# Kernel tuning notes

Measured on AMD Instinct MI355X. Metric: run time of the kernel, lower is better.

Reference implementation:

```python
import jax, jax.numpy as jnp
import numpy as np

N_NODES = 100000
IN_F = 32
OUT_F = 32
EDGE_F = 16
N_EDGES = 400000
BN_EPS = 1e-5
LEAKY_SLOPE = 0.01


def setup_inputs() -> dict:
    key = jax.random.key(0)
    ks = jax.random.split(key, 8)
    node_feature = jax.random.normal(ks[0], (N_NODES, IN_F), dtype=jnp.float32)
    edge_feature = jax.random.normal(ks[1], (N_EDGES, EDGE_F), dtype=jnp.float32)
    nn_w = jax.random.normal(ks[2], (EDGE_F, IN_F * OUT_F), dtype=jnp.float32) * (1.0 / np.sqrt(EDGE_F))
    nn_b = jax.random.normal(ks[3], (IN_F * OUT_F,), dtype=jnp.float32) * 0.01
    root = jax.random.normal(ks[4], (IN_F, OUT_F), dtype=jnp.float32) * (1.0 / np.sqrt(IN_F))
    bias = jax.random.normal(ks[5], (OUT_F,), dtype=jnp.float32) * 0.01
    gamma = jnp.ones((OUT_F,), dtype=jnp.float32)
    beta = jnp.zeros((OUT_F,), dtype=jnp.float32)
    edge_index = jax.random.randint(ks[6], (2, N_EDGES), 0, N_NODES, dtype=jnp.int64)
    return {
        "node_feature": node_feature,
        "edge_feature": edge_feature,
        "nn_w": nn_w,
        "nn_b": nn_b,
        "root": root,
        "bias": bias,
        "gamma": gamma,
        "beta": beta,
        "edge_index": edge_index,
    }


def reference(node_feature, edge_feature, nn_w, nn_b, root, bias, gamma, beta, edge_index):
    src, dst = edge_index[0], edge_index[1]  # messages flow src -> dst (PyG source_to_target)
    # Edge MLP: per-edge weight matrix [E, IN_F, OUT_F]
    edge_w = (edge_feature @ nn_w + nn_b).reshape(-1, IN_F, OUT_F)
    # Gather source node features and apply per-edge matmul: [E, OUT_F]
    msg = jnp.einsum("ei,eio->eo", node_feature[src], edge_w)
    # Scatter-add aggregation at target nodes
    agg = jax.ops.segment_sum(msg, dst, num_segments=node_feature.shape[0])
    # Root transform + bias (NNConv root_weight=True, bias=True)
    h = agg + node_feature @ root + bias
    # BatchNorm1d (training mode: batch statistics over nodes, biased variance)
    mean = jnp.mean(h, axis=0)
    var = jnp.var(h, axis=0)
    h = (h - mean) * jax.lax.rsqrt(var + BN_EPS) * gamma + beta
    # LeakyReLU (default negative_slope = 0.01)
    return jnp.where(h >= 0, h, LEAKY_SLOPE * h)
```

## Files before the change

### kernel.cpp

```cpp
#include <hip/hip_runtime.h>

#define IN_F 32
#define OUT_F 32
#define EDGE_F 16
#define BN_EPS 1e-5f
#define SLOPE 0.01f

typedef _Float16 half_t;
typedef __attribute__((ext_vector_type(4))) _Float16 h4;
typedef __attribute__((ext_vector_type(8))) _Float16 f16x8;
typedef __attribute__((ext_vector_type(4))) float f32x4;

#define BCOLS 576
#define BSTRIDE_B 80

__global__ __launch_bounds__(256) void prep_bt_kernel(
    const float* __restrict__ W, const float* __restrict__ b,
    const float* __restrict__ root, half_t* __restrict__ BtG) {
  int idx = blockIdx.x * 256 + threadIdx.x;
  if (idx >= BCOLS * 32) return;
  int o = idx & 31;
  int k = (idx >> 5) & 31;
  int fp = idx >> 10;
  float v;
  int col;
  if (fp < 16) {
    v = W[(size_t)fp * 1024 + k * 32 + o];
    col = fp * 32 + o;
  } else if (fp == 16) {
    v = b[k * 32 + o];
    col = 512 + o;
  } else {
    v = root[k * 32 + o];
    col = 544 + o;
  }
  BtG[(size_t)col * 32 + k] = (half_t)v;
}

__global__ __launch_bounds__(256) void gemm_y_mfma_kernel(
    const float* __restrict__ x, const half_t* __restrict__ BtG,
    const float* __restrict__ bias, half_t* __restrict__ Y,
    float* __restrict__ out, int N) {
  __shared__ char BtL[BCOLS * BSTRIDE_B];

  int tid = threadIdx.x;
  for (int t = tid; t < BCOLS * 4; t += 256) {
    int col = t >> 2, part = t & 3;
    *(float4*)(BtL + col * BSTRIDE_B + part * 16) =
        *(const float4*)((const char*)BtG + col * 64 + part * 16);
  }
  __syncthreads();

  int wv = tid >> 6, lane = tid & 63;
  int lr = lane & 15, kg = lane >> 4;
  int n0 = blockIdx.x * 64 + wv * 16;
  int row = n0 + lr;

  f16x8 a;
  if (row < N) {
    float4 u0 = *(const float4*)(x + (size_t)row * 32 + kg * 8);
    float4 u1 = *(const float4*)(x + (size_t)row * 32 + kg * 8 + 4);
    a[0] = (half_t)u0.x; a[1] = (half_t)u0.y; a[2] = (half_t)u0.z; a[3] = (half_t)u0.w;
    a[4] = (half_t)u1.x; a[5] = (half_t)u1.y; a[6] = (half_t)u1.z; a[7] = (half_t)u1.w;
  } else {
    a = (f16x8)(half_t)0.f;
  }

  for (int ct = 0; ct < 36; ++ct) {
    int col = ct * 16 + lr;
    f16x8 bf = *(const f16x8*)(BtL + col * BSTRIDE_B + kg * 16);
    f32x4 c = {0.f, 0.f, 0.f, 0.f};
    c = __builtin_amdgcn_mfma_f32_16x16x32_f16(a, bf, c, 0, 0, 0);
    if (col < 544) {
#pragma unroll
      for (int j = 0; j < 4; ++j) {
        int n = n0 + kg * 4 + j;
        if (n < N) Y[(size_t)n * 544 + col] = (half_t)c[j];
      }
    } else {
      int o = col - 544;
      float bv = bias[o];
#pragma unroll
      for (int j = 0; j < 4; ++j) {
        int n = n0 + kg * 4 + j;
        if (n < N) out[(size_t)n * OUT_F + o] = c[j] + bv;
      }
    }
  }
}

__global__ __launch_bounds__(256) void edge_light_kernel(
    const half_t* __restrict__ Y, const float* __restrict__ ef,
    const int* __restrict__ ei, float* __restrict__ agg, int E) {
  __shared__ float efl[32][17];
  __shared__ float msg[32][33];
  __shared__ int dstl[32];

  int e0 = blockIdx.x * 32;
  int t = threadIdx.x;
  int el = t >> 3, oq = t & 7;
  int e = e0 + el;
  bool ev = (e < E);
  int s = ev ? ei[e] : 0;

  const half_t* yrow = Y + (size_t)s * 544 + oq * 4;
  h4 yv[17];
#pragma unroll
  for (int f = 0; f < 17; ++f) yv[f] = *(const h4*)(yrow + f * 32);
  __builtin_amdgcn_sched_barrier(0);

  if (t < 128) {
    int ee = e0 + (t >> 2);
    int q = t & 3;
    float4 v = make_float4(0.f, 0.f, 0.f, 0.f);
    if (ee < E) v = *(const float4*)(ef + (size_t)ee * EDGE_F + q * 4);
    efl[t >> 2][q * 4 + 0] = v.x; efl[t >> 2][q * 4 + 1] = v.y;
    efl[t >> 2][q * 4 + 2] = v.z; efl[t >> 2][q * 4 + 3] = v.w;
  }
  if (t < 32) {
    int ee = e0 + t;
    dstl[t] = (ee < E) ? ei[E + ee] : -1;
  }
  __syncthreads();

  float acc[4];
#pragma unroll
  for (int j = 0; j < 4; ++j) acc[j] = (float)yv[16][j];
#pragma unroll
  for (int f = 0; f < EDGE_F; ++f) {
    float m = efl[el][f];
#pragma unroll
    for (int j = 0; j < 4; ++j) acc[j] = fmaf(m, (float)yv[f][j], acc[j]);
  }
#pragma unroll
  for (int j = 0; j < 4; ++j) msg[el][oq * 4 + j] = acc[j];
  __syncthreads();

  int d = dstl[el];
  if (d >= 0) {
    float* dp = agg + (size_t)d * OUT_F;
#pragma unroll
    for (int j = 0; j < 4; ++j)
      atomicAdd(dp + j * 8 + oq, msg[el][j * 8 + oq]);
  }
}

__global__ __launch_bounds__(256) void node_root_kernel(
    const float* __restrict__ x, const float* __restrict__ root,
    const float* __restrict__ bias, float* __restrict__ agg, int N) {
  __shared__ float rl[IN_F * OUT_F];
  __shared__ float bl[OUT_F];
  for (int t = threadIdx.x; t < IN_F * OUT_F; t += blockDim.x) rl[t] = root[t];
  if (threadIdx.x < OUT_F) bl[threadIdx.x] = bias[threadIdx.x];
  __syncthreads();
  int n = blockIdx.x * blockDim.x + threadIdx.x;
  bool valid = (n < N);
  int nu = valid ? n : 0;
  float xr[IN_F];
  const float4* xp = (const float4*)(x + (size_t)nu * IN_F);
#pragma unroll
  for (int q = 0; q < IN_F / 4; ++q) {
    float4 v = xp[q];
    xr[q * 4 + 0] = v.x; xr[q * 4 + 1] = v.y; xr[q * 4 + 2] = v.z; xr[q * 4 + 3] = v.w;
  }
  float acc[OUT_F];
#pragma unroll
  for (int o = 0; o < OUT_F; ++o) acc[o] = bl[o];
#pragma unroll
  for (int i = 0; i < IN_F; ++i) {
    float xi = xr[i];
#pragma unroll
    for (int o = 0; o < OUT_F; ++o) acc[o] = fmaf(xi, rl[i * OUT_F + o], acc[o]);
  }
  if (valid) {
    float4* op = (float4*)(agg + (size_t)n * OUT_F);
#pragma unroll
    for (int q = 0; q < OUT_F / 4; ++q)
      op[q] = make_float4(acc[q * 4 + 0], acc[q * 4 + 1], acc[q * 4 + 2], acc[q * 4 + 3]);
  }
}

__global__ __launch_bounds__(256) void edge_kernel(
    const float* __restrict__ x, const float* __restrict__ ef,
    const float* __restrict__ W, const float* __restrict__ b,
    const int* __restrict__ ei, float* __restrict__ agg, int E) {
  __shared__ float Wl[EDGE_F * IN_F * OUT_F];
  int e = blockIdx.x * blockDim.x + threadIdx.x;
  bool valid = (e < E);
  int eu = valid ? e : 0;
  int s = ei[eu];
  int d = ei[E + eu];
  float efr[EDGE_F];
  {
    const float4* ep = (const float4*)(ef + (size_t)eu * EDGE_F);
#pragma unroll
    for (int q = 0; q < EDGE_F / 4; ++q) {
      float4 v = ep[q];
      efr[q * 4 + 0] = v.x; efr[q * 4 + 1] = v.y;
      efr[q * 4 + 2] = v.z; efr[q * 4 + 3] = v.w;
    }
  }
  const float* xrow = x + (size_t)s * IN_F;
  float acc[OUT_F];
#pragma unroll
  for (int o = 0; o < OUT_F; ++o) acc[o] = 0.f;
  for (int t = threadIdx.x; t < IN_F * OUT_F; t += 256) Wl[t] = b[t];
  __syncthreads();
  for (int i = 0; i < IN_F; ++i) {
    float xi = xrow[i];
    const float* br = &Wl[i * OUT_F];
#pragma unroll
    for (int o = 0; o < OUT_F; ++o) acc[o] = fmaf(xi, br[o], acc[o]);
  }
  __syncthreads();
  for (int t = threadIdx.x; t < EDGE_F * IN_F * OUT_F / 4; t += 256)
    ((float4*)Wl)[t] = ((const float4*)W)[t];
  __syncthreads();
  for (int i = 0; i < IN_F; ++i) {
    float xi = xrow[i];
#pragma unroll
    for (int f = 0; f < EDGE_F; ++f) {
      float m = efr[f] * xi;
      const float* wr = &Wl[(f * IN_F + i) * OUT_F];
#pragma unroll
      for (int o = 0; o < OUT_F; ++o) acc[o] = fmaf(m, wr[o], acc[o]);
    }
  }
  if (valid) {
    float* dp = agg + (size_t)d * OUT_F;
#pragma unroll
    for (int o = 0; o < OUT_F; ++o) atomicAdd(dp + o, acc[o]);
  }
}

__global__ __launch_bounds__(256) void bn_stats_kernel(
    const float* __restrict__ h, float* __restrict__ stats, int total) {
  int t = blockIdx.x * blockDim.x + threadIdx.x;
  int stride = gridDim.x * blockDim.x;
  float s = 0.f, s2 = 0.f;
  for (int idx = t; idx < total; idx += stride) {
    float v = h[idx];
    s += v;
    s2 = fmaf(v, v, s2);
  }
  __shared__ float ls[256], ls2[256];
  ls[threadIdx.x] = s;
  ls2[threadIdx.x] = s2;
  __syncthreads();
  if (threadIdx.x < 32) {
    float a = ls[threadIdx.x], a2 = ls2[threadIdx.x];
    for (int j = 32 + threadIdx.x; j < 256; j += 32) { a += ls[j]; a2 += ls2[j]; }
    atomicAdd(&stats[threadIdx.x], a);
    atomicAdd(&stats[32 + threadIdx.x], a2);
  }
}

__global__ __launch_bounds__(256) void bn_apply_kernel(
    float* __restrict__ h, const float* __restrict__ stats,
    const float* __restrict__ gamma, const float* __restrict__ beta,
    int total, float invN) {
  int t = blockIdx.x * blockDim.x + threadIdx.x;
  int i4 = t * 4;
  if (i4 >= total) return;
  float4 v = *(const float4*)(h + i4);
  float r[4] = {v.x, v.y, v.z, v.w};
  int o0 = i4 & 31;
#pragma unroll
  for (int j = 0; j < 4; ++j) {
    int o = o0 + j;
    float m = stats[o] * invN;
    float var = fmaf(-m, m, stats[32 + o] * invN);
    float sc = rsqrtf(var + BN_EPS) * gamma[o];
    float val = (r[j] - m) * sc + beta[o];
    r[j] = val >= 0.f ? val : SLOPE * val;
  }
  *(float4*)(h + i4) = make_float4(r[0], r[1], r[2], r[3]);
}

extern "C" void kernel_launch(void* const* d_in, const int* in_sizes, int n_in,
                              void* d_out, int out_size, void* d_ws, size_t ws_size,
                              hipStream_t stream) {
  const float* x     = (const float*)d_in[0];
  const float* ef    = (const float*)d_in[1];
  const float* W     = (const float*)d_in[2];
  const float* b     = (const float*)d_in[3];
  const float* root  = (const float*)d_in[4];
  const float* bias  = (const float*)d_in[5];
  const float* gamma = (const float*)d_in[6];
  const float* beta  = (const float*)d_in[7];
  const int*   ei    = (const int*)d_in[8];

  float* out = (float*)d_out;
  float* stats = (float*)d_ws;
  half_t* BtG = (half_t*)((char*)d_ws + 1024);
  half_t* Y = (half_t*)((char*)d_ws + 1024 + 36864);

  int N = in_sizes[0] / IN_F;
  int E = in_sizes[1] / EDGE_F;
  int total = N * OUT_F;
  size_t need = 1024 + 36864 + (size_t)N * 544 * sizeof(half_t);

  hipMemsetAsync(stats, 0, 64 * sizeof(float), stream);

  if (ws_size >= need) {
    prep_bt_kernel<<<(BCOLS * 32 + 255) / 256, 256, 0, stream>>>(W, b, root, BtG);
    gemm_y_mfma_kernel<<<(N + 63) / 64, 256, 0, stream>>>(x, BtG, bias, Y, out, N);
    edge_light_kernel<<<(E + 31) / 32, 256, 0, stream>>>(Y, ef, ei, out, E);
  } else {
    node_root_kernel<<<(N + 255) / 256, 256, 0, stream>>>(x, root, bias, out, N);
    edge_kernel<<<(E + 255) / 256, 256, 0, stream>>>(x, ef, W, b, ei, out, E);
  }
  bn_stats_kernel<<<1024, 256, 0, stream>>>(out, stats, total);
  bn_apply_kernel<<<(total / 4 + 255) / 256, 256, 0, stream>>>(out, stats, gamma, beta, total, 1.0f / (float)N);
}
```

Baseline: 180.3 us.

## Bucket-sort edges by source node and remap blocks across XCDs for gather locality

After: 242.2 us. 1.34x slower.

```diff
diff --git a/kernel.cpp b/kernel.cpp
--- a/kernel.cpp
+++ b/kernel.cpp
@@ -5,6 +5,7 @@
 #define EDGE_F 16
 #define BN_EPS 1e-5f
 #define SLOPE 0.01f
+#define NBUCKET 128
 
 typedef _Float16 half_t;
 typedef __attribute__((ext_vector_type(4))) _Float16 h4;
@@ -16,7 +17,12 @@
 
 __global__ __launch_bounds__(256) void prep_bt_kernel(
     const float* __restrict__ W, const float* __restrict__ b,
-    const float* __restrict__ root, half_t* __restrict__ BtG) {
+    const float* __restrict__ root, half_t* __restrict__ BtG,
+    float* __restrict__ stats, int* __restrict__ hist) {
+  if (blockIdx.x == 0) {
+    if (threadIdx.x < 64) stats[threadIdx.x] = 0.f;
+    else if (threadIdx.x < 64 + NBUCKET) hist[threadIdx.x - 64] = 0;
+  }
   int idx = blockIdx.x * 256 + threadIdx.x;
   if (idx >= BCOLS * 32) return;
   int o = idx & 31;
@@ -37,6 +43,49 @@
   BtG[(size_t)col * 32 + k] = (half_t)v;
 }
 
+__global__ __launch_bounds__(256) void hist_kernel(
+    const int* __restrict__ ei, int* __restrict__ hist, int E, int shift) {
+  __shared__ int lh[NBUCKET];
+  if (threadIdx.x < NBUCKET) lh[threadIdx.x] = 0;
+  __syncthreads();
+  int e = blockIdx.x * 256 + threadIdx.x;
+  if (e < E) atomicAdd(&lh[ei[e] >> shift], 1);
+  __syncthreads();
+  if (threadIdx.x < NBUCKET && lh[threadIdx.x] > 0)
+    atomicAdd(&hist[threadIdx.x], lh[threadIdx.x]);
+}
+
+__global__ __launch_bounds__(256) void scan_kernel(
+    const int* __restrict__ hist, int* __restrict__ cursor) {
+  if (threadIdx.x == 0) {
+    int acc = 0;
+    for (int i = 0; i < NBUCKET; ++i) {
+      cursor[i] = acc;
+      acc += hist[i];
+    }
+  }
+}
+
+__global__ __launch_bounds__(256) void scatter_kernel(
+    const int* __restrict__ ei, int* __restrict__ cursor,
+    int* __restrict__ perm, int E, int shift) {
+  __shared__ int lh[NBUCKET];
+  __shared__ int lbase[NBUCKET];
+  if (threadIdx.x < NBUCKET) lh[threadIdx.x] = 0;
+  __syncthreads();
+  int e = blockIdx.x * 256 + threadIdx.x;
+  int bkt = 0, rank = 0;
+  if (e < E) {
+    bkt = ei[e] >> shift;
+    rank = atomicAdd(&lh[bkt], 1);
+  }
+  __syncthreads();
+  if (threadIdx.x < NBUCKET && lh[threadIdx.x] > 0)
+    lbase[threadIdx.x] = atomicAdd(&cursor[threadIdx.x], lh[threadIdx.x]);
+  __syncthreads();
+  if (e < E) perm[lbase[bkt] + rank] = e;
+}
+
 __global__ __launch_bounds__(256) void gemm_y_mfma_kernel(
     const float* __restrict__ x, const half_t* __restrict__ BtG,
     const float* __restrict__ bias, half_t* __restrict__ Y,
@@ -91,17 +140,24 @@
 
 __global__ __launch_bounds__(256) void edge_light_kernel(
     const half_t* __restrict__ Y, const float* __restrict__ ef,
-    const int* __restrict__ ei, float* __restrict__ agg, int E) {
+    const int* __restrict__ ei, const int* __restrict__ perm,
+    float* __restrict__ agg, int E) {
+  int nwg = gridDim.x;
+  int xcd = blockIdx.x & 7, off = blockIdx.x >> 3;
+  int q = nwg >> 3, r = nwg & 7;
+  int bid = (xcd < r) ? xcd * (q + 1) + off : r * (q + 1) + (xcd - r) * q + off;
+
   __shared__ float efl[32][17];
   __shared__ float msg[32][33];
   __shared__ int dstl[32];
 
-  int e0 = blockIdx.x * 32;
+  int e0 = bid * 32;
   int t = threadIdx.x;
   int el = t >> 3, oq = t & 7;
   int e = e0 + el;
   bool ev = (e < E);
-  int s = ev ? ei[e] : 0;
+  int pe = ev ? perm[e] : 0;
+  int s = ev ? ei[pe] : 0;
 
   const half_t* yrow = Y + (size_t)s * 544 + oq * 4;
   h4 yv[17];
@@ -110,16 +166,16 @@
   __builtin_amdgcn_sched_barrier(0);
 
   if (t < 128) {
-    int ee = e0 + (t >> 2);
-    int q = t & 3;
+    int ep = e0 + (t >> 2);
+    int qq = t & 3;
     float4 v = make_float4(0.f, 0.f, 0.f, 0.f);
-    if (ee < E) v = *(const float4*)(ef + (size_t)ee * EDGE_F + q * 4);
-    efl[t >> 2][q * 4 + 0] = v.x; efl[t >> 2][q * 4 + 1] = v.y;
-    efl[t >> 2][q * 4 + 2] = v.z; efl[t >> 2][q * 4 + 3] = v.w;
+    if (ep < E) v = *(const float4*)(ef + (size_t)perm[ep] * EDGE_F + qq * 4);
+    efl[t >> 2][qq * 4 + 0] = v.x; efl[t >> 2][qq * 4 + 1] = v.y;
+    efl[t >> 2][qq * 4 + 2] = v.z; efl[t >> 2][qq * 4 + 3] = v.w;
   }
   if (t < 32) {
-    int ee = e0 + t;
-    dstl[t] = (ee < E) ? ei[E + ee] : -1;
+    int ep = e0 + t;
+    dstl[t] = (ep < E) ? ei[E + perm[ep]] : -1;
   }
   __syncthreads();
 
@@ -290,23 +346,34 @@
   const float* beta  = (const float*)d_in[7];
   const int*   ei    = (const int*)d_in[8];
 
-  float* out = (float*)d_out;
-  float* stats = (float*)d_ws;
-  half_t* BtG = (half_t*)((char*)d_ws + 1024);
-  half_t* Y = (half_t*)((char*)d_ws + 1024 + 36864);
-
   int N = in_sizes[0] / IN_F;
   int E = in_sizes[1] / EDGE_F;
   int total = N * OUT_F;
-  size_t need = 1024 + 36864 + (size_t)N * 544 * sizeof(half_t);
-
-  hipMemsetAsync(stats, 0, 64 * sizeof(float), stream);
+
+  float* out = (float*)d_out;
+  char* wsb = (char*)d_ws;
+  float*  stats  = (float*)wsb;
+  half_t* BtG    = (half_t*)(wsb + 1024);
+  int*    hist   = (int*)(wsb + 1024 + 36864);
+  int*    cursor = (int*)(wsb + 1024 + 36864 + 512);
+  int*    perm   = (int*)(wsb + 1024 + 36864 + 1024);
+  size_t yoff = 1024 + 36864 + 1024 + (((size_t)E * 4 + 1023) & ~(size_t)1023);
+  half_t* Y = (half_t*)(wsb + yoff);
+
+  int shift = 10;
+  while (((N - 1) >> shift) >= NBUCKET) ++shift;
+
+  size_t need = yoff + (size_t)N * 544 * sizeof(half_t);
 
   if (ws_size >= need) {
-    prep_bt_kernel<<<(BCOLS * 32 + 255) / 256, 256, 0, stream>>>(W, b, root, BtG);
+    prep_bt_kernel<<<(BCOLS * 32 + 255) / 256, 256, 0, stream>>>(W, b, root, BtG, stats, hist);
+    hist_kernel<<<(E + 255) / 256, 256, 0, stream>>>(ei, hist, E, shift);
+    scan_kernel<<<1, 256, 0, stream>>>(hist, cursor);
+    scatter_kernel<<<(E + 255) / 256, 256, 0, stream>>>(ei, cursor, perm, E, shift);
     gemm_y_mfma_kernel<<<(N + 63) / 64, 256, 0, stream>>>(x, BtG, bias, Y, out, N);
-    edge_light_kernel<<<(E + 31) / 32, 256, 0, stream>>>(Y, ef, ei, out, E);
+    edge_light_kernel<<<(E + 31) / 32, 256, 0, stream>>>(Y, ef, ei, perm, out, E);
   } else {
+    hipMemsetAsync(stats, 0, 64 * sizeof(float), stream);
     node_root_kernel<<<(N + 255) / 256, 256, 0, stream>>>(x, root, bias, out, N);
     edge_kernel<<<(E + 255) / 256, 256, 0, stream>>>(x, ef, W, b, ei, out, E);
   }
```

## Replace atomic scatter with CSR-sorted gather aggregation and coalesced GEMM stores

Applied to the files above, without the earlier changes.

Result: slower. 222.3 us (+23.3%).

```diff
diff --git a/kernel.cpp b/kernel.cpp
--- a/kernel.cpp
+++ b/kernel.cpp
@@ -37,11 +37,65 @@
   BtG[(size_t)col * 32 + k] = (half_t)v;
 }
 
+__global__ __launch_bounds__(256) void histd_kernel(
+    const int* __restrict__ ei, int* __restrict__ cnt, int E) {
+  int e = blockIdx.x * 256 + threadIdx.x;
+  if (e < E) atomicAdd(&cnt[ei[E + e]], 1);
+}
+
+__global__ __launch_bounds__(256) void scan_a_kernel(
+    const int* __restrict__ cnt, int* __restrict__ rp, int* __restrict__ bsum, int N) {
+  __shared__ int lds[256];
+  int i = blockIdx.x * 256 + threadIdx.x;
+  int v = (i < N) ? cnt[i] : 0;
+  lds[threadIdx.x] = v;
+  __syncthreads();
+  int ex = 0;
+  for (int j = 0; j < threadIdx.x; ++j) ex += lds[j];
+  if (i < N) rp[i] = ex;
+  if (threadIdx.x == 255) bsum[blockIdx.x] = ex + v;
+}
+
+__global__ __launch_bounds__(512) void scan_b_kernel(
+    const int* __restrict__ bsum, int* __restrict__ bcur, int nb) {
+  __shared__ int lds[512];
+  int t = threadIdx.x;
+  lds[t] = (t < nb) ? bsum[t] : 0;
+  __syncthreads();
+  int ex = 0;
+  for (int j = 0; j < t; ++j) ex += lds[j];
+  if (t < nb) bcur[t] = ex;
+}
+
+__global__ __launch_bounds__(256) void scan_c_kernel(
+    int* __restrict__ rp, int* __restrict__ cursor,
+    const int* __restrict__ bcur, int N, int E) {
+  int i = blockIdx.x * 256 + threadIdx.x;
+  if (i < N) {
+    int v = rp[i] + bcur[i >> 8];
+    rp[i] = v;
+    cursor[i] = v;
+  }
+  if (i == 0) rp[N] = E;
+}
+
+__global__ __launch_bounds__(256) void scatterd_kernel(
+    const int* __restrict__ ei, int* __restrict__ cursor,
+    int* __restrict__ permd, int E) {
+  int e = blockIdx.x * 256 + threadIdx.x;
+  if (e < E) {
+    int d = ei[E + e];
+    int r = atomicAdd(&cursor[d], 1);
+    permd[r] = e;
+  }
+}
+
 __global__ __launch_bounds__(256) void gemm_y_mfma_kernel(
     const float* __restrict__ x, const half_t* __restrict__ BtG,
     const float* __restrict__ bias, half_t* __restrict__ Y,
     float* __restrict__ out, int N) {
   __shared__ char BtL[BCOLS * BSTRIDE_B];
+  __shared__ float tile[4][16][18];
 
   int tid = threadIdx.x;
   for (int t = tid; t < BCOLS * 4; t += 256) {
@@ -66,35 +120,41 @@
     a = (f16x8)(half_t)0.f;
   }
 
+  int rr = lane & 15, qq = lane >> 4;
+  int nst = n0 + rr;
+
   for (int ct = 0; ct < 36; ++ct) {
     int col = ct * 16 + lr;
     f16x8 bf = *(const f16x8*)(BtL + col * BSTRIDE_B + kg * 16);
     f32x4 c = {0.f, 0.f, 0.f, 0.f};
     c = __builtin_amdgcn_mfma_f32_16x16x32_f16(a, bf, c, 0, 0, 0);
-    if (col < 544) {
-#pragma unroll
-      for (int j = 0; j < 4; ++j) {
-        int n = n0 + kg * 4 + j;
-        if (n < N) Y[(size_t)n * 544 + col] = (half_t)c[j];
-      }
-    } else {
-      int o = col - 544;
-      float bv = bias[o];
-#pragma unroll
-      for (int j = 0; j < 4; ++j) {
-        int n = n0 + kg * 4 + j;
-        if (n < N) out[(size_t)n * OUT_F + o] = c[j] + bv;
+#pragma unroll
+    for (int j = 0; j < 4; ++j) tile[wv][kg * 4 + j][lr] = c[j];
+    __builtin_amdgcn_wave_barrier();
+    if (nst < N) {
+      float v0 = tile[wv][rr][qq * 4 + 0];
+      float v1 = tile[wv][rr][qq * 4 + 1];
+      float v2 = tile[wv][rr][qq * 4 + 2];
+      float v3 = tile[wv][rr][qq * 4 + 3];
+      if (ct < 34) {
+        h4 hv;
+        hv[0] = (half_t)v0; hv[1] = (half_t)v1; hv[2] = (half_t)v2; hv[3] = (half_t)v3;
+        *(h4*)(Y + (size_t)nst * 544 + ct * 16 + qq * 4) = hv;
+      } else {
+        int o = (ct - 34) * 16 + qq * 4;
+        float4 bv = *(const float4*)(bias + o);
+        *(float4*)(out + (size_t)nst * OUT_F + o) =
+            make_float4(v0 + bv.x, v1 + bv.y, v2 + bv.z, v3 + bv.w);
       }
     }
-  }
-}
-
-__global__ __launch_bounds__(256) void edge_light_kernel(
+    __builtin_amdgcn_wave_barrier();
+  }
+}
+
+__global__ __launch_bounds__(256) void edge_msg_kernel(
     const half_t* __restrict__ Y, const float* __restrict__ ef,
-    const int* __restrict__ ei, float* __restrict__ agg, int E) {
+    const int* __restrict__ ei, half_t* __restrict__ msg, int E) {
   __shared__ float efl[32][17];
-  __shared__ float msg[32][33];
-  __shared__ int dstl[32];
 
   int e0 = blockIdx.x * 32;
   int t = threadIdx.x;
@@ -106,22 +166,24 @@
   const half_t* yrow = Y + (size_t)s * 544 + oq * 4;
   h4 yv[17];
 #pragma unroll
-  for (int f = 0; f < 17; ++f) yv[f] = *(const h4*)(yrow + f * 32);
-  __builtin_amdgcn_sched_barrier(0);
+  for (int f = 0; f < 17; ++f) {
+    asm volatile("global_load_dwordx2 %0, %1, off offset:%2"
+                 : "=v"(yv[f])
+                 : "v"(yrow), "i"(f * 64));
+  }
 
   if (t < 128) {
     int ee = e0 + (t >> 2);
-    int q = t & 3;
+    int qq = t & 3;
     float4 v = make_float4(0.f, 0.f, 0.f, 0.f);
-    if (ee < E) v = *(const float4*)(ef + (size_t)ee * EDGE_F + q * 4);
-    efl[t >> 2][q * 4 + 0] = v.x; efl[t >> 2][q * 4 + 1] = v.y;
-    efl[t >> 2][q * 4 + 2] = v.z; efl[t >> 2][q * 4 + 3] = v.w;
-  }
-  if (t < 32) {
-    int ee = e0 + t;
-    dstl[t] = (ee < E) ? ei[E + ee] : -1;
-  }
-  __syncthreads();
+    if (ee < E) v = *(const float4*)(ef + (size_t)ee * EDGE_F + qq * 4);
+    efl[t >> 2][qq * 4 + 0] = v.x; efl[t >> 2][qq * 4 + 1] = v.y;
+    efl[t >> 2][qq * 4 + 2] = v.z; efl[t >> 2][qq * 4 + 3] = v.w;
+  }
+  __syncthreads();
+
+  asm volatile("s_waitcnt vmcnt(0)" ::: "memory");
+  __builtin_amdgcn_sched_barrier(0);
 
   float acc[4];
 #pragma unroll
@@ -132,17 +194,30 @@
 #pragma unroll
     for (int j = 0; j < 4; ++j) acc[j] = fmaf(m, (float)yv[f][j], acc[j]);
   }
-#pragma unroll
-  for (int j = 0; j < 4; ++j) msg[el][oq * 4 + j] = acc[j];
-  __syncthreads();
-
-  int d = dstl[el];
-  if (d >= 0) {
-    float* dp = agg + (size_t)d * OUT_F;
-#pragma unroll
-    for (int j = 0; j < 4; ++j)
-      atomicAdd(dp + j * 8 + oq, msg[el][j * 8 + oq]);
-  }
+
+  if (ev) {
+    h4 hv;
+    hv[0] = (half_t)acc[0]; hv[1] = (half_t)acc[1];
+    hv[2] = (half_t)acc[2]; hv[3] = (half_t)acc[3];
+    *(h4*)(msg + (size_t)e * 32 + oq * 4) = hv;
+  }
+}
+
+__global__ __launch_bounds__(256) void node_agg_kernel(
+    const half_t* __restrict__ msg, const int* __restrict__ rp,
+    const int* __restrict__ permd, float* __restrict__ out, int N) {
+  int g = threadIdx.x >> 3, oq = threadIdx.x & 7;
+  int n = blockIdx.x * 32 + g;
+  if (n >= N) return;
+  int kb = rp[n], ke = rp[n + 1];
+  float4 acc = *(const float4*)(out + (size_t)n * 32 + oq * 4);
+  for (int k = kb; k < ke; ++k) {
+    int e = permd[k];
+    h4 v = *(const h4*)(msg + (size_t)e * 32 + oq * 4);
+    acc.x += (float)v[0]; acc.y += (float)v[1];
+    acc.z += (float)v[2]; acc.w += (float)v[3];
+  }
+  *(float4*)(out + (size_t)n * 32 + oq * 4) = acc;
 }
 
 __global__ __launch_bounds__(256) void node_root_kernel(
@@ -290,23 +365,42 @@
   const float* beta  = (const float*)d_in[7];
   const int*   ei    = (const int*)d_in[8];
 
-  float* out = (float*)d_out;
-  float* stats = (float*)d_ws;
-  half_t* BtG = (half_t*)((char*)d_ws + 1024);
-  half_t* Y = (half_t*)((char*)d_ws + 1024 + 36864);
-
   int N = in_sizes[0] / IN_F;
   int E = in_sizes[1] / EDGE_F;
   int total = N * OUT_F;
-  size_t need = 1024 + 36864 + (size_t)N * 544 * sizeof(half_t);
-
-  hipMemsetAsync(stats, 0, 64 * sizeof(float), stream);
-
-  if (ws_size >= need) {
+  int nb = (N + 255) / 256;
+
+  float* out = (float*)d_out;
+  char* wsb = (char*)d_ws;
+
+  size_t off = 0;
+  auto alloc = [&](size_t bytes) { size_t o = off; off = (off + bytes + 1023) & ~(size_t)1023; return o; };
+  float*  stats  = (float*)(wsb + alloc(256));
+  half_t* BtG    = (half_t*)(wsb + alloc(BCOLS * 32 * sizeof(half_t)));
+  int*    cnt    = (int*)(wsb + alloc((size_t)N * 4));
+  int*    rp     = (int*)(wsb + alloc((size_t)(N + 1) * 4));
+  int*    cursor = (int*)(wsb + alloc((size_t)N * 4));
+  int*    bsum   = (int*)(wsb + alloc((size_t)nb * 4));
+  int*    bcur   = (int*)(wsb + alloc((size_t)nb * 4));
+  int*    permd  = (int*)(wsb + alloc((size_t)E * 4));
+  half_t* msg    = (half_t*)(wsb + alloc((size_t)E * 32 * sizeof(half_t)));
+  half_t* Y      = (half_t*)(wsb + alloc((size_t)N * 544 * sizeof(half_t)));
+  size_t need = off;
+
+  if (ws_size >= need && nb <= 512) {
+    hipMemsetAsync(stats, 0, 256, stream);
+    hipMemsetAsync(cnt, 0, (size_t)N * 4, stream);
     prep_bt_kernel<<<(BCOLS * 32 + 255) / 256, 256, 0, stream>>>(W, b, root, BtG);
+    histd_kernel<<<(E + 255) / 256, 256, 0, stream>>>(ei, cnt, E);
+    scan_a_kernel<<<nb, 256, 0, stream>>>(cnt, rp, bsum, N);
+    scan_b_kernel<<<1, 512, 0, stream>>>(bsum, bcur, nb);
+    scan_c_kernel<<<nb, 256, 0, stream>>>(rp, cursor, bcur, N, E);
+    scatterd_kernel<<<(E + 255) / 256, 256, 0, stream>>>(ei, cursor, permd, E);
     gemm_y_mfma_kernel<<<(N + 63) / 64, 256, 0, stream>>>(x, BtG, bias, Y, out, N);
-    edge_light_kernel<<<(E + 31) / 32, 256, 0, stream>>>(Y, ef, ei, out, E);
+    edge_msg_kernel<<<(E + 31) / 32, 256, 0, stream>>>(Y, ef, ei, msg, E);
+    node_agg_kernel<<<(N + 31) / 32, 256, 0, stream>>>(msg, rp, permd, out, N);
   } else {
+    hipMemsetAsync(stats, 0, 256, stream);
     node_root_kernel<<<(N + 255) / 256, 256, 0, stream>>>(x, root, bias, out, N);
     edge_kernel<<<(E + 255) / 256, 256, 0, stream>>>(x, ef, W, b, ei, out, E);
   }
```
